# Optimization experiments

Measured on AMD Instinct MI355X. Metric: run time of the kernel, lower is better.

The kernel has to match this reference:

```python
import jax, jax.numpy as jnp
import numpy as np

B, S, H, NH = 2, 2048, 1024, 16
PH = H // NH  # per-head size = 64


def setup_inputs() -> dict:
    key = jax.random.key(0)
    ks = jax.random.split(key, 12)
    scale = 0.02
    inp = {
        "key": jax.random.normal(ks[0], (B, S, H), jnp.float32),
        "value": jax.random.normal(ks[1], (B, S, H), jnp.float32),
        "query": jax.random.normal(ks[2], (B, S, H), jnp.float32),
        "mask": jax.random.uniform(ks[3], (B, 1, S, S), jnp.float32),
        "i": 0,
        "Wq": jax.random.normal(ks[4], (H, H), jnp.float32) * scale,
        "bq": jnp.zeros((H,), jnp.float32),
        "Wk": jax.random.normal(ks[5], (H, H), jnp.float32) * scale,
        "bk": jnp.zeros((H,), jnp.float32),
        "Wv": jax.random.normal(ks[6], (H, H), jnp.float32) * scale,
        "bv": jnp.zeros((H,), jnp.float32),
        "Wo": jax.random.normal(ks[7], (H, H), jnp.float32) * scale,
        "bo": jnp.zeros((H,), jnp.float32),
    }
    return inp


def reference(key, value, query, mask, i, Wq, bq, Wk, bk, Wv, bv, Wo, bo):
    # Linear projections (torch nn.Linear: x @ W.T + b), then split heads -> [B, NH, S, PH]
    def proj(x, W, b):
        return (x @ W.T + b).reshape(B, S, NH, PH).transpose(0, 2, 1, 3)

    q = proj(query, Wq, bq)
    k = proj(key, Wk, bk)
    v = proj(value, Wv, bv)

    # scores: [B, NH, S, S]; scale then MULTIPLICATIVE mask (as in the original)
    scores = jnp.einsum('bhqd,bhkd->bhqk', q, k) / jnp.sqrt(jnp.float32(PH))
    scores = scores * mask
    probs = jax.nn.softmax(scores, axis=-1)  # dropout p=0 -> identity

    # context: [B, NH, S, PH] -> merge heads -> [B, S, H]
    ctx = jnp.einsum('bhqk,bhkd->bhqd', probs, v)
    ctx = ctx.transpose(0, 2, 1, 3).reshape(B, S, H)
    return ctx @ Wo.T + bo
```

## Files before the change

### kernel.cpp

```cpp
#include <hip/hip_runtime.h>

typedef unsigned short ushort_t;
typedef __attribute__((ext_vector_type(8))) __bf16 bf16x8;
typedef __attribute__((ext_vector_type(4))) float f32x4;

__device__ inline float bf2f(ushort_t u) {
  union { unsigned int i; float f; } v; v.i = ((unsigned int)u) << 16; return v.f;
}
__device__ inline ushort_t f2bf(float f) {
  union { float f; unsigned int i; } v; v.f = f;
  unsigned int r = (v.i + 0x7fffu + ((v.i >> 16) & 1u)) >> 16;
  return (ushort_t)r;
}

__global__ void detect_dtype_kernel(const ushort_t* __restrict__ w,
                                    int* __restrict__ flag) {
  if (threadIdx.x == 0 && blockIdx.x == 0) {
    int sane = 0;
    for (int i = 0; i < 256; i++) {
      float a = fabsf(bf2f(w[i]));
      if (a >= 1e-4f && a <= 0.5f) sane++;
    }
    *flag = (sane >= 192) ? 1 : 0;
  }
}

__device__ inline void stage8(ushort_t* dst, const void* src, size_t idx, int isbf) {
  if (isbf) {
    *(bf16x8*)dst = *(const bf16x8*)((const ushort_t*)src + idx);
  } else {
    const float* s = (const float*)src + idx;
    float4 a = *(const float4*)s;
    float4 b = *(const float4*)(s + 4);
    union { bf16x8 v; ushort_t u[8]; } t;
    t.u[0] = f2bf(a.x); t.u[1] = f2bf(a.y); t.u[2] = f2bf(a.z); t.u[3] = f2bf(a.w);
    t.u[4] = f2bf(b.x); t.u[5] = f2bf(b.y); t.u[6] = f2bf(b.z); t.u[7] = f2bf(b.w);
    *(bf16x8*)dst = t.v;
  }
}

__device__ inline float ld1(const void* src, size_t idx, int isbf) {
  return isbf ? bf2f(((const ushort_t*)src)[idx]) : ((const float*)src)[idx];
}

#define BM 128
#define BN 128
#define BK 32
#define KDIM 1024
#define NDIM 1024

template <int MODE>
__device__ inline void gemm_body(const void* __restrict__ X,
                                 const void* __restrict__ W,
                                 const void* __restrict__ Bias,
                                 void* __restrict__ Out,
                                 int xbf, int wbf, int obf) {
  __shared__ ushort_t As[BM][BK + 8];
  __shared__ ushort_t Bs[BN][BK + 8];
  const int tid = threadIdx.x;
  const int wave = tid >> 6, lane = tid & 63;
  const int g = lane >> 4, l16 = lane & 15;
  const int m0 = blockIdx.y * BM, n0 = blockIdx.x * BN;
  const int wm = (wave >> 1) * 64, wn = (wave & 1) * 64;

  f32x4 acc[4][4] = {};
  const int r0 = tid >> 2, c0 = (tid & 3) * 8;

  for (int k0 = 0; k0 < KDIM; k0 += BK) {
    stage8(&As[r0][c0],      X, (size_t)(m0 + r0) * KDIM + k0 + c0, xbf);
    stage8(&As[r0 + 64][c0], X, (size_t)(m0 + r0 + 64) * KDIM + k0 + c0, xbf);
    stage8(&Bs[r0][c0],      W, (size_t)(n0 + r0) * KDIM + k0 + c0, wbf);
    stage8(&Bs[r0 + 64][c0], W, (size_t)(n0 + r0 + 64) * KDIM + k0 + c0, wbf);
    __syncthreads();
    bf16x8 af[4], bfr[4];
    for (int i = 0; i < 4; i++) af[i]  = *(const bf16x8*)&As[wm + i * 16 + l16][g * 8];
    for (int j = 0; j < 4; j++) bfr[j] = *(const bf16x8*)&Bs[wn + j * 16 + l16][g * 8];
    for (int i = 0; i < 4; i++)
      for (int j = 0; j < 4; j++)
        acc[i][j] = __builtin_amdgcn_mfma_f32_16x16x32_bf16(af[i], bfr[j], acc[i][j], 0, 0, 0);
    __syncthreads();
  }
  for (int i = 0; i < 4; i++)
    for (int j = 0; j < 4; j++)
      for (int r = 0; r < 4; r++) {
        int m = m0 + wm + i * 16 + g * 4 + r;
        int n = n0 + wn + j * 16 + l16;
        float v = acc[i][j][r] + ld1(Bias, n, wbf);
        if (MODE == 0) {
          if (obf) ((ushort_t*)Out)[(size_t)m * NDIM + n] = f2bf(v);
          else     ((float*)Out)[(size_t)m * NDIM + n] = v;
        } else {
          int b = m >> 11, s = m & 2047, h = n >> 6, d = n & 63;
          ((ushort_t*)Out)[((((size_t)b * 16 + h) * 2048) + s) * 64 + d] = f2bf(v);
        }
      }
}

__global__ __launch_bounds__(256) void proj_qkv_kernel(
    const void* __restrict__ query, const void* __restrict__ key,
    const void* __restrict__ value,
    const void* __restrict__ Wq, const void* __restrict__ bq,
    const void* __restrict__ Wk, const void* __restrict__ bk,
    const void* __restrict__ Wv, const void* __restrict__ bv,
    ushort_t* __restrict__ Q, ushort_t* __restrict__ K, ushort_t* __restrict__ V,
    const int* __restrict__ flag) {
  int f = *flag;
  int z = blockIdx.z;
  const void* X = z == 0 ? query : z == 1 ? key : value;
  const void* W = z == 0 ? Wq : z == 1 ? Wk : Wv;
  const void* B = z == 0 ? bq : z == 1 ? bk : bv;
  ushort_t* O  = z == 0 ? Q  : z == 1 ? K  : V;
  gemm_body<1>(X, W, B, O, f, f, 1);
}

__global__ __launch_bounds__(256) void out_proj_kernel(
    const ushort_t* __restrict__ X, const void* __restrict__ W,
    const void* __restrict__ B, void* __restrict__ O,
    const int* __restrict__ flag) {
  int f = *flag;
  gemm_body<0>(X, W, B, O, 1, f, f);
}

#define FS 70

__global__ __launch_bounds__(256, 4) void flash_attn_kernel(
    const ushort_t* __restrict__ Q, const ushort_t* __restrict__ K,
    const ushort_t* __restrict__ V, const void* __restrict__ mask,
    ushort_t* __restrict__ ctx, const int* __restrict__ flag) {
  __shared__ ushort_t Qs[64][FS];
  __shared__ ushort_t Ks[64][FS];
  __shared__ ushort_t Vt[64][FS];
  __shared__ ushort_t Ps[4][16][FS];

  const int f = *flag;
  const int tid = threadIdx.x;
  const int wave = tid >> 6, lane = tid & 63;
  const int g = lane >> 4, l16 = lane & 15;
  const int bh = blockIdx.x;
  const int b = bh >> 4, h = bh & 15;
  const int q0 = blockIdx.y * 64;

  const ushort_t* Qh = Q + (size_t)bh * 2048 * 64;
  const ushort_t* Kh = K + (size_t)bh * 2048 * 64;
  const ushort_t* Vh = V + (size_t)bh * 2048 * 64;
  const size_t mrow0 = (size_t)b * 2048 * 2048 + (size_t)q0 * 2048;

  const int r = tid >> 2, c = (tid & 3) * 16;
  {
    *(bf16x8*)&Qs[r][c]     = *(const bf16x8*)&Qh[(size_t)(q0 + r) * 64 + c];
    *(bf16x8*)&Qs[r][c + 8] = *(const bf16x8*)&Qh[(size_t)(q0 + r) * 64 + c + 8];
  }
  __syncthreads();
  const bf16x8 aq0 = *(const bf16x8*)&Qs[wave * 16 + l16][g * 8];
  const bf16x8 aq1 = *(const bf16x8*)&Qs[wave * 16 + l16][32 + g * 8];

  float lpart[4] = {0.f, 0.f, 0.f, 0.f};
  f32x4 o_acc[4] = {};
  const int mrow = wave * 16 + g * 4;

  for (int kt0 = 0; kt0 < 2048; kt0 += 64) {
    {
      *(bf16x8*)&Ks[r][c]     = *(const bf16x8*)&Kh[(size_t)(kt0 + r) * 64 + c];
      *(bf16x8*)&Ks[r][c + 8] = *(const bf16x8*)&Kh[(size_t)(kt0 + r) * 64 + c + 8];
      union { bf16x8 v; ushort_t u[8]; } a0, a1;
      a0.v = *(const bf16x8*)&Vh[(size_t)(kt0 + r) * 64 + c];
      a1.v = *(const bf16x8*)&Vh[(size_t)(kt0 + r) * 64 + c + 8];
      for (int i = 0; i < 8; i++) Vt[c + i][r] = a0.u[i];
      for (int i = 0; i < 8; i++) Vt[c + 8 + i][r] = a1.u[i];
    }
    float mv[4][4];
    if (f) {
      const ushort_t* mp = (const ushort_t*)mask;
      for (int j = 0; j < 4; j++)
        for (int rr = 0; rr < 4; rr++)
          mv[j][rr] = bf2f(mp[mrow0 + (size_t)(mrow + rr) * 2048 + kt0 + j * 16 + l16]);
    } else {
      const float* mp = (const float*)mask;
      for (int j = 0; j < 4; j++)
        for (int rr = 0; rr < 4; rr++)
          mv[j][rr] = mp[mrow0 + (size_t)(mrow + rr) * 2048 + kt0 + j * 16 + l16];
    }
    __syncthreads();

    f32x4 sc[4] = {};
    for (int j = 0; j < 4; j++) {
      bf16x8 bk0 = *(const bf16x8*)&Ks[j * 16 + l16][g * 8];
      bf16x8 bk1 = *(const bf16x8*)&Ks[j * 16 + l16][32 + g * 8];
      sc[j] = __builtin_amdgcn_mfma_f32_16x16x32_bf16(aq0, bk0, sc[j], 0, 0, 0);
      sc[j] = __builtin_amdgcn_mfma_f32_16x16x32_bf16(aq1, bk1, sc[j], 0, 0, 0);
    }

    for (int j = 0; j < 4; j++)
      for (int rr = 0; rr < 4; rr++) {
        float s = fminf(sc[j][rr] * 0.125f * mv[j][rr], 80.f);
        float p = __expf(s);
        unsigned int pb = __float_as_uint(p);
        lpart[rr] += __uint_as_float(pb & 0xffff0000u);
        Ps[wave][g * 4 + rr][j * 16 + l16] = (ushort_t)(pb >> 16);
      }
    __syncthreads();

    bf16x8 pf0 = *(const bf16x8*)&Ps[wave][l16][g * 8];
    bf16x8 pf1 = *(const bf16x8*)&Ps[wave][l16][32 + g * 8];
    for (int jd = 0; jd < 4; jd++) {
      bf16x8 vf0 = *(const bf16x8*)&Vt[jd * 16 + l16][g * 8];
      bf16x8 vf1 = *(const bf16x8*)&Vt[jd * 16 + l16][32 + g * 8];
      o_acc[jd] = __builtin_amdgcn_mfma_f32_16x16x32_bf16(pf0, vf0, o_acc[jd], 0, 0, 0);
      o_acc[jd] = __builtin_amdgcn_mfma_f32_16x16x32_bf16(pf1, vf1, o_acc[jd], 0, 0, 0);
    }
    __syncthreads();
  }

  float rl[4];
  for (int rr = 0; rr < 4; rr++) {
    float l = lpart[rr];
    l += __shfl_xor(l, 1, 64);
    l += __shfl_xor(l, 2, 64);
    l += __shfl_xor(l, 4, 64);
    l += __shfl_xor(l, 8, 64);
    rl[rr] = 1.0f / l;
  }
  for (int jd = 0; jd < 4; jd++)
    for (int rr = 0; rr < 4; rr++) {
      int qrow = q0 + mrow + rr;
      ctx[((size_t)b * 2048 + qrow) * 1024 + h * 64 + jd * 16 + l16] =
          f2bf(o_acc[jd][rr] * rl[rr]);
    }
}

extern "C" void kernel_launch(void* const* d_in, const int* in_sizes, int n_in,
                              void* d_out, int out_size, void* d_ws, size_t ws_size,
                              hipStream_t stream) {
  (void)in_sizes; (void)n_in; (void)out_size; (void)ws_size;
  const void* key   = d_in[0];
  const void* value = d_in[1];
  const void* query = d_in[2];
  const void* mask  = d_in[3];
  const void* Wq = d_in[5];
  const void* bq = d_in[6];
  const void* Wk = d_in[7];
  const void* bk = d_in[8];
  const void* Wv = d_in[9];
  const void* bv = d_in[10];
  const void* Wo = d_in[11];
  const void* bo = d_in[12];

  const size_t E = (size_t)2 * 2048 * 1024;
  ushort_t* Qw  = (ushort_t*)d_ws;
  ushort_t* Kw  = Qw + E;
  ushort_t* Vw  = Kw + E;
  ushort_t* CTX = Vw + E;
  int* flag = (int*)(CTX + E);

  detect_dtype_kernel<<<1, 64, 0, stream>>>((const ushort_t*)Wq, flag);
  proj_qkv_kernel<<<dim3(8, 32, 3), 256, 0, stream>>>(query, key, value,
                                                      Wq, bq, Wk, bk, Wv, bv,
                                                      Qw, Kw, Vw, flag);
  flash_attn_kernel<<<dim3(32, 32), 256, 0, stream>>>(Qw, Kw, Vw, mask, CTX, flag);
  out_proj_kernel<<<dim3(8, 32), 256, 0, stream>>>(CTX, Wo, bo, d_out, flag);
}
```

Measured before the change: 407.7 us.

## Prefetch GEMM and attention tiles into registers and pre-transpose V

The GEMM main loop now loads the next K-slice into registers while the current one is computed. The attention loop double-buffers K, V and mask loads in registers and drops one block barrier, relying on each wave reading only its own probability rows. A separate kernel pre-transposes V into workspace when enough workspace exists, and Q is pre-scaled by 1/8. The changes aim to hide global latency and remove the strided LDS transpose, at the cost of more registers, an extra launch and extra workspace traffic.

Result: slower. 475.0 us (+16.5%).

```diff
diff --git a/kernel.cpp b/kernel.cpp
--- a/kernel.cpp
+++ b/kernel.cpp
@@ -25,22 +25,32 @@
   }
 }
 
-__device__ inline void stage8(ushort_t* dst, const void* src, size_t idx, int isbf) {
+__device__ inline float ld1(const void* src, size_t idx, int isbf) {
+  return isbf ? bf2f(((const ushort_t*)src)[idx]) : ((const float*)src)[idx];
+}
+
+struct pre8 { float4 a, b; };
+__device__ inline pre8 pref8(const void* src, size_t idx, int isbf) {
+  pre8 u;
   if (isbf) {
-    *(bf16x8*)dst = *(const bf16x8*)((const ushort_t*)src + idx);
+    u.a = *(const float4*)((const ushort_t*)src + idx);
+    u.b = u.a;
   } else {
     const float* s = (const float*)src + idx;
-    float4 a = *(const float4*)s;
-    float4 b = *(const float4*)(s + 4);
-    union { bf16x8 v; ushort_t u[8]; } t;
-    t.u[0] = f2bf(a.x); t.u[1] = f2bf(a.y); t.u[2] = f2bf(a.z); t.u[3] = f2bf(a.w);
-    t.u[4] = f2bf(b.x); t.u[5] = f2bf(b.y); t.u[6] = f2bf(b.z); t.u[7] = f2bf(b.w);
+    u.a = *(const float4*)s;
+    u.b = *(const float4*)(s + 4);
+  }
+  return u;
+}
+__device__ inline void commit8(ushort_t* dst, pre8 u, int isbf) {
+  if (isbf) {
+    *(float4*)dst = u.a;
+  } else {
+    union { bf16x8 v; ushort_t u8[8]; } t;
+    t.u8[0] = f2bf(u.a.x); t.u8[1] = f2bf(u.a.y); t.u8[2] = f2bf(u.a.z); t.u8[3] = f2bf(u.a.w);
+    t.u8[4] = f2bf(u.b.x); t.u8[5] = f2bf(u.b.y); t.u8[6] = f2bf(u.b.z); t.u8[7] = f2bf(u.b.w);
     *(bf16x8*)dst = t.v;
   }
-}
-
-__device__ inline float ld1(const void* src, size_t idx, int isbf) {
-  return isbf ? bf2f(((const ushort_t*)src)[idx]) : ((const float*)src)[idx];
 }
 
 #define BM 128
@@ -66,11 +76,24 @@
   f32x4 acc[4][4] = {};
   const int r0 = tid >> 2, c0 = (tid & 3) * 8;
 
+  const size_t ia0 = (size_t)(m0 + r0) * KDIM + c0;
+  const size_t ia1 = (size_t)(m0 + r0 + 64) * KDIM + c0;
+  const size_t ib0 = (size_t)(n0 + r0) * KDIM + c0;
+  const size_t ib1 = (size_t)(n0 + r0 + 64) * KDIM + c0;
+
+  pre8 pa0 = pref8(X, ia0, xbf), pa1 = pref8(X, ia1, xbf);
+  pre8 pb0 = pref8(W, ib0, wbf), pb1 = pref8(W, ib1, wbf);
+
   for (int k0 = 0; k0 < KDIM; k0 += BK) {
-    stage8(&As[r0][c0],      X, (size_t)(m0 + r0) * KDIM + k0 + c0, xbf);
-    stage8(&As[r0 + 64][c0], X, (size_t)(m0 + r0 + 64) * KDIM + k0 + c0, xbf);
-    stage8(&Bs[r0][c0],      W, (size_t)(n0 + r0) * KDIM + k0 + c0, wbf);
-    stage8(&Bs[r0 + 64][c0], W, (size_t)(n0 + r0 + 64) * KDIM + k0 + c0, wbf);
+    commit8(&As[r0][c0],      pa0, xbf);
+    commit8(&As[r0 + 64][c0], pa1, xbf);
+    commit8(&Bs[r0][c0],      pb0, wbf);
+    commit8(&Bs[r0 + 64][c0], pb1, wbf);
+    const int kn = k0 + BK;
+    if (kn < KDIM) {
+      pa0 = pref8(X, ia0 + kn, xbf); pa1 = pref8(X, ia1 + kn, xbf);
+      pb0 = pref8(W, ib0 + kn, wbf); pb1 = pref8(W, ib1 + kn, wbf);
+    }
     __syncthreads();
     bf16x8 af[4], bfr[4];
     for (int i = 0; i < 4; i++) af[i]  = *(const bf16x8*)&As[wm + i * 16 + l16][g * 8];
@@ -121,15 +144,35 @@
   gemm_body<0>(X, W, B, O, 1, f, f);
 }
 
-#define FS 70
-
+__global__ __launch_bounds__(256) void transpose_v_kernel(
+    const ushort_t* __restrict__ Vin, ushort_t* __restrict__ Vout) {
+  __shared__ ushort_t T[64][72];
+  const int tid = threadIdx.x;
+  const int r = tid >> 2, c = (tid & 3) * 16;
+  const int bh = blockIdx.y;
+  const int s0 = blockIdx.x * 64;
+  const ushort_t* src = Vin + (size_t)bh * 2048 * 64;
+  *(bf16x8*)&T[r][c]     = *(const bf16x8*)&src[(size_t)(s0 + r) * 64 + c];
+  *(bf16x8*)&T[r][c + 8] = *(const bf16x8*)&src[(size_t)(s0 + r) * 64 + c + 8];
+  __syncthreads();
+  union { bf16x8 v; ushort_t u[8]; } o0, o1;
+  for (int i = 0; i < 8; i++) o0.u[i] = T[c + i][r];
+  for (int i = 0; i < 8; i++) o1.u[i] = T[c + 8 + i][r];
+  ushort_t* dst = Vout + (size_t)bh * 64 * 2048;
+  *(bf16x8*)&dst[(size_t)r * 2048 + s0 + c]     = o0.v;
+  *(bf16x8*)&dst[(size_t)r * 2048 + s0 + c + 8] = o1.v;
+}
+
+#define FS 72
+
+template <int PRET>
 __global__ __launch_bounds__(256, 4) void flash_attn_kernel(
     const ushort_t* __restrict__ Q, const ushort_t* __restrict__ K,
     const ushort_t* __restrict__ V, const void* __restrict__ mask,
     ushort_t* __restrict__ ctx, const int* __restrict__ flag) {
   __shared__ ushort_t Qs[64][FS];
   __shared__ ushort_t Ks[64][FS];
-  __shared__ ushort_t Vt[64][FS];
+  __shared__ ushort_t Vs[64][FS];
   __shared__ ushort_t Ps[4][16][FS];
 
   const int f = *flag;
@@ -142,13 +185,23 @@
 
   const ushort_t* Qh = Q + (size_t)bh * 2048 * 64;
   const ushort_t* Kh = K + (size_t)bh * 2048 * 64;
-  const ushort_t* Vh = V + (size_t)bh * 2048 * 64;
+  const ushort_t* Vh = PRET ? V + (size_t)bh * 64 * 2048
+                            : V + (size_t)bh * 2048 * 64;
   const size_t mrow0 = (size_t)b * 2048 * 2048 + (size_t)q0 * 2048;
+  const int mrow = wave * 16 + g * 4;
 
   const int r = tid >> 2, c = (tid & 3) * 16;
+
   {
-    *(bf16x8*)&Qs[r][c]     = *(const bf16x8*)&Qh[(size_t)(q0 + r) * 64 + c];
-    *(bf16x8*)&Qs[r][c + 8] = *(const bf16x8*)&Qh[(size_t)(q0 + r) * 64 + c + 8];
+    union { bf16x8 v; ushort_t u[8]; } a0, a1;
+    a0.v = *(const bf16x8*)&Qh[(size_t)(q0 + r) * 64 + c];
+    a1.v = *(const bf16x8*)&Qh[(size_t)(q0 + r) * 64 + c + 8];
+    for (int i = 0; i < 8; i++) {
+      a0.u[i] = f2bf(bf2f(a0.u[i]) * 0.125f);
+      a1.u[i] = f2bf(bf2f(a1.u[i]) * 0.125f);
+    }
+    *(bf16x8*)&Qs[r][c]     = a0.v;
+    *(bf16x8*)&Qs[r][c + 8] = a1.v;
   }
   __syncthreads();
   const bf16x8 aq0 = *(const bf16x8*)&Qs[wave * 16 + l16][g * 8];
@@ -156,29 +209,53 @@
 
   float lpart[4] = {0.f, 0.f, 0.f, 0.f};
   f32x4 o_acc[4] = {};
-  const int mrow = wave * 16 + g * 4;
-
-  for (int kt0 = 0; kt0 < 2048; kt0 += 64) {
-    {
-      *(bf16x8*)&Ks[r][c]     = *(const bf16x8*)&Kh[(size_t)(kt0 + r) * 64 + c];
-      *(bf16x8*)&Ks[r][c + 8] = *(const bf16x8*)&Kh[(size_t)(kt0 + r) * 64 + c + 8];
-      union { bf16x8 v; ushort_t u[8]; } a0, a1;
-      a0.v = *(const bf16x8*)&Vh[(size_t)(kt0 + r) * 64 + c];
-      a1.v = *(const bf16x8*)&Vh[(size_t)(kt0 + r) * 64 + c + 8];
-      for (int i = 0; i < 8; i++) Vt[c + i][r] = a0.u[i];
-      for (int i = 0; i < 8; i++) Vt[c + 8 + i][r] = a1.u[i];
-    }
-    float mv[4][4];
+
+  bf16x8 kr0, kr1, vr0, vr1;
+  auto pref_kv = [&](int kt0) {
+    kr0 = *(const bf16x8*)&Kh[(size_t)(kt0 + r) * 64 + c];
+    kr1 = *(const bf16x8*)&Kh[(size_t)(kt0 + r) * 64 + c + 8];
+    if (PRET) {
+      vr0 = *(const bf16x8*)&Vh[(size_t)r * 2048 + kt0 + c];
+      vr1 = *(const bf16x8*)&Vh[(size_t)r * 2048 + kt0 + c + 8];
+    } else {
+      vr0 = *(const bf16x8*)&Vh[(size_t)(kt0 + r) * 64 + c];
+      vr1 = *(const bf16x8*)&Vh[(size_t)(kt0 + r) * 64 + c + 8];
+    }
+  };
+  auto pref_mask = [&](int kt0, float* mv) {
     if (f) {
       const ushort_t* mp = (const ushort_t*)mask;
       for (int j = 0; j < 4; j++)
         for (int rr = 0; rr < 4; rr++)
-          mv[j][rr] = bf2f(mp[mrow0 + (size_t)(mrow + rr) * 2048 + kt0 + j * 16 + l16]);
+          mv[j * 4 + rr] = bf2f(mp[mrow0 + (size_t)(mrow + rr) * 2048 + kt0 + j * 16 + l16]);
     } else {
       const float* mp = (const float*)mask;
       for (int j = 0; j < 4; j++)
         for (int rr = 0; rr < 4; rr++)
-          mv[j][rr] = mp[mrow0 + (size_t)(mrow + rr) * 2048 + kt0 + j * 16 + l16];
+          mv[j * 4 + rr] = mp[mrow0 + (size_t)(mrow + rr) * 2048 + kt0 + j * 16 + l16];
+    }
+  };
+
+  float mvA[16], mvB[16];
+  pref_kv(0);
+  pref_mask(0, mvA);
+
+  auto step = [&](int kt0, float* cur, float* nxt) {
+    __syncthreads();
+    *(bf16x8*)&Ks[r][c]     = kr0;
+    *(bf16x8*)&Ks[r][c + 8] = kr1;
+    if (PRET) {
+      *(bf16x8*)&Vs[r][c]     = vr0;
+      *(bf16x8*)&Vs[r][c + 8] = vr1;
+    } else {
+      union { bf16x8 v; ushort_t u[8]; } a0, a1;
+      a0.v = vr0; a1.v = vr1;
+      for (int i = 0; i < 8; i++) Vs[c + i][r] = a0.u[i];
+      for (int i = 0; i < 8; i++) Vs[c + 8 + i][r] = a1.u[i];
+    }
+    if (kt0 + 64 < 2048) {
+      pref_kv(kt0 + 64);
+      pref_mask(kt0 + 64, nxt);
     }
     __syncthreads();
 
@@ -192,23 +269,27 @@
 
     for (int j = 0; j < 4; j++)
       for (int rr = 0; rr < 4; rr++) {
-        float s = fminf(sc[j][rr] * 0.125f * mv[j][rr], 80.f);
+        float s = fminf(sc[j][rr] * cur[j * 4 + rr], 80.f);
         float p = __expf(s);
         unsigned int pb = __float_as_uint(p);
         lpart[rr] += __uint_as_float(pb & 0xffff0000u);
         Ps[wave][g * 4 + rr][j * 16 + l16] = (ushort_t)(pb >> 16);
       }
-    __syncthreads();
+    asm volatile("" ::: "memory");
 
     bf16x8 pf0 = *(const bf16x8*)&Ps[wave][l16][g * 8];
     bf16x8 pf1 = *(const bf16x8*)&Ps[wave][l16][32 + g * 8];
     for (int jd = 0; jd < 4; jd++) {
-      bf16x8 vf0 = *(const bf16x8*)&Vt[jd * 16 + l16][g * 8];
-      bf16x8 vf1 = *(const bf16x8*)&Vt[jd * 16 + l16][32 + g * 8];
+      bf16x8 vf0 = *(const bf16x8*)&Vs[jd * 16 + l16][g * 8];
+      bf16x8 vf1 = *(const bf16x8*)&Vs[jd * 16 + l16][32 + g * 8];
       o_acc[jd] = __builtin_amdgcn_mfma_f32_16x16x32_bf16(pf0, vf0, o_acc[jd], 0, 0, 0);
       o_acc[jd] = __builtin_amdgcn_mfma_f32_16x16x32_bf16(pf1, vf1, o_acc[jd], 0, 0, 0);
     }
-    __syncthreads();
+  };
+
+  for (int kt0 = 0; kt0 < 2048; kt0 += 128) {
+    step(kt0,      mvA, mvB);
+    step(kt0 + 64, mvB, mvA);
   }
 
   float rl[4];
@@ -231,7 +312,7 @@
 extern "C" void kernel_launch(void* const* d_in, const int* in_sizes, int n_in,
                               void* d_out, int out_size, void* d_ws, size_t ws_size,
                               hipStream_t stream) {
-  (void)in_sizes; (void)n_in; (void)out_size; (void)ws_size;
+  (void)in_sizes; (void)n_in; (void)out_size;
   const void* key   = d_in[0];
   const void* value = d_in[1];
   const void* query = d_in[2];
@@ -251,11 +332,19 @@
   ushort_t* Vw  = Kw + E;
   ushort_t* CTX = Vw + E;
   int* flag = (int*)(CTX + E);
+  ushort_t* Vt = (ushort_t*)((char*)(CTX + E) + 256);
+
+  const int pret = (ws_size >= 4 * E * 2 + 256 + E * 2) ? 1 : 0;
 
   detect_dtype_kernel<<<1, 64, 0, stream>>>((const ushort_t*)Wq, flag);
   proj_qkv_kernel<<<dim3(8, 32, 3), 256, 0, stream>>>(query, key, value,
                                                       Wq, bq, Wk, bk, Wv, bv,
                                                       Qw, Kw, Vw, flag);
-  flash_attn_kernel<<<dim3(32, 32), 256, 0, stream>>>(Qw, Kw, Vw, mask, CTX, flag);
+  if (pret) {
+    transpose_v_kernel<<<dim3(32, 32), 256, 0, stream>>>(Vw, Vt);
+    flash_attn_kernel<1><<<dim3(32, 32), 256, 0, stream>>>(Qw, Kw, Vt, mask, CTX, flag);
+  } else {
+    flash_attn_kernel<0><<<dim3(32, 32), 256, 0, stream>>>(Qw, Kw, Vw, mask, CTX, flag);
+  }
   out_proj_kernel<<<dim3(8, 32), 256, 0, stream>>>(CTX, Wo, bo, d_out, flag);
 }
```
